# Performance work log

Hardware: AMD Instinct MI355X
Metric: run time of the kernel (lower is better)

The kernel has to match this reference:

```python
import jax, jax.numpy as jnp
import numpy as np
from jax import lax

B, H, W = 16, 512, 512
K, C, D = 64, 512, 256  # num_clusters, feature channels, descriptor_dim


def conv2d(x, w, b, stride, pad):
    y = lax.conv_general_dilated(x, w, (stride, stride), ((pad, pad), (pad, pad)),
                                 dimension_numbers=("NCHW", "OIHW", "NCHW"))
    return y + b[None, :, None, None]


def maxpool2(x):
    return lax.reduce_window(x, -jnp.inf, lax.max, (1, 1, 2, 2), (1, 1, 2, 2), "VALID")


def setup_inputs() -> dict:
    key = jax.random.key(0)
    ks = jax.random.split(key, 16)
    def rn(k, shape, fan_in):
        return jax.random.normal(k, shape, jnp.float32) * (1.0 / np.sqrt(fan_in))
    return {
        "x": jax.random.normal(ks[0], (B, 3, H, W), jnp.float32),
        "w1": rn(ks[1], (64, 3, 3, 3), 27), "b1": jnp.zeros((64,), jnp.float32),
        "w2": rn(ks[2], (128, 64, 3, 3), 576), "b2": jnp.zeros((128,), jnp.float32),
        "w3": rn(ks[3], (256, 128, 3, 3), 1152), "b3": jnp.zeros((256,), jnp.float32),
        "w4": rn(ks[4], (512, 256, 3, 3), 2304), "b4": jnp.zeros((512,), jnp.float32),
        "wv": rn(ks[5], (K, C), C), "bv": jnp.zeros((K,), jnp.float32),
        "centroids": jax.random.normal(ks[6], (K, C), jnp.float32),
        "fw1": rn(ks[7], (D, K * C), K * C), "fb1": jnp.zeros((D,), jnp.float32),
        "fw2": rn(ks[8], (D, D), D), "fb2": jnp.zeros((D,), jnp.float32),
    }


def reference(x, w1, b1, w2, b2, w3, b3, w4, b4, wv, bv, centroids, fw1, fb1, fw2, fb2):
    # conv backbone (SimpleGlobalDescriptor.backbone)
    h = jax.nn.relu(conv2d(x, w1, b1, 2, 1)); h = maxpool2(h)
    h = jax.nn.relu(conv2d(h, w2, b2, 2, 1)); h = maxpool2(h)
    h = jax.nn.relu(conv2d(h, w3, b3, 2, 1)); h = maxpool2(h)
    h = jax.nn.relu(conv2d(h, w4, b4, 2, 1))
    feats = jnp.mean(h, axis=(2, 3))  # AdaptiveAvgPool2d((1,1)) -> (B, C)
    # NetVLAD soft assignment: 1x1 conv + softmax over cluster dim
    logits = jnp.einsum("bc,kc->bk", feats, wv) + bv  # (B, K)
    a = jax.nn.softmax(logits, axis=1)  # spatial N == 1 after avgpool
    # fused VLAD: a[:,k] * (feats - centroids[k]) summed over N(=1)
    # == a (outer) feats - a[:,:,None] * centroids
    vlad = a[:, :, None] * (feats[:, None, :] - centroids[None, :, :])  # (B, K, C)
    v = vlad.reshape(B, K * C)
    # final descriptor MLP + L2 norm
    d = jax.nn.relu(v @ fw1.T + fb1) @ fw2.T + fb2
    d = d / jnp.linalg.norm(d, axis=1, keepdims=True)
    return d
```

## Files before the change

kernel.cpp:

```cpp
#include <hip/hip_runtime.h>
#include <hip/hip_bf16.h>

typedef unsigned short ushort_t;
typedef short bf16x8 __attribute__((ext_vector_type(8)));
typedef float f32x4 __attribute__((ext_vector_type(4)));

__device__ __forceinline__ ushort_t f2b(float f) {
    __hip_bfloat16 h = __float2bfloat16(f);
    return *reinterpret_cast<ushort_t*>(&h);
}
__device__ __forceinline__ float b2f(short v) {
    union { unsigned int u; float f; } cv;
    cv.u = ((unsigned int)(ushort_t)v) << 16;
    return cv.f;
}

__global__ __launch_bounds__(256) void k_packall(const float* __restrict__ w1,
                                                 const float* __restrict__ w2,
                                                 const float* __restrict__ w3,
                                                 const float* __restrict__ w4,
                                                 ushort_t* __restrict__ o1,
                                                 ushort_t* __restrict__ o2,
                                                 ushort_t* __restrict__ o3,
                                                 ushort_t* __restrict__ o4m) {
    const int bx = blockIdx.x;
    if (bx < 512) {
        const int co = bx;
        __shared__ float sw[2304];
        for (int i = threadIdx.x; i < 2304; i += 256) sw[i] = w4[(size_t)co * 2304 + i];
        __syncthreads();
        const int g = co >> 4, l15 = co & 15;
        for (int it = threadIdx.x; it < 288; it += 256) {
            const int kc = it >> 2, kg = it & 3;
            const int k0 = kc * 32 + kg * 8;
            const int tap = k0 >> 8, ci0 = k0 & 255;
            const int lane = kg * 16 + l15;
            ushort_t tmp[8];
#pragma unroll
            for (int j = 0; j < 8; ++j)
                tmp[j] = f2b(sw[(ci0 + j) * 9 + tap]);
            *(float4*)(o4m + ((size_t)(kc * 32 + g) * 64 + lane) * 8) = *(const float4*)tmp;
        }
    } else if (bx < 656) {
        const int slot = (bx - 512) * 256 + threadIdx.x;
        const int lane = slot & 63, g = (slot >> 6) & 15, kc = slot >> 10;
        const int k0 = kc * 32 + ((lane >> 4) << 3);
        const int tap = k0 >> 7, cib = k0 & 127;
        const int ky = tap >= 6 ? 2 : (tap >= 3 ? 1 : 0), kx = tap - ky * 3;
        const int co = g * 16 + (lane & 15);
#pragma unroll
        for (int j = 0; j < 8; ++j)
            o3[slot * 8 + j] = f2b(w3[((co * 128 + cib + j) * 3 + ky) * 3 + kx]);
    } else if (bx < 692) {
        const int slot = (bx - 656) * 256 + threadIdx.x;
        const int lane = slot & 63, g = (slot >> 6) & 7, kc = slot >> 9;
        const int k0 = kc * 32 + ((lane >> 4) << 3);
        const int tap = k0 >> 6, sb = k0 & 63;
        const int ky = tap >= 6 ? 2 : (tap >= 3 ? 1 : 0), kx = tap - ky * 3;
        const int co = g * 16 + (lane & 15);
#pragma unroll
        for (int j = 0; j < 8; ++j) {
            const int s = sb + j;
            const int ci = 16 * (s & 3) + (s >> 2);
            o2[slot * 8 + j] = f2b(w2[((co * 64 + ci) * 3 + ky) * 3 + kx]);
        }
    } else {
        const int slot = threadIdx.x;
        const int lane = slot & 63, nf = slot >> 6;
        const int co = nf * 16 + (lane & 15);
        const int kg = lane >> 4;
#pragma unroll
        for (int j = 0; j < 8; ++j) {
            const int k = kg * 8 + j;
            float v = 0.f;
            if (k < 24) {
                const int ky = k >> 3, q = k & 7;
                const int kx = q / 3, c = q - 3 * kx;
                v = w1[(co * 3 + c) * 9 + ky * 3 + kx];
            } else if (k < 27) {
                const int ky = k - 24;
                v = w1[(co * 3 + 2) * 9 + ky * 3 + 2];
            }
            o1[slot * 8 + j] = f2b(v);
        }
    }
}

__global__ __launch_bounds__(256) void k_conv1f(const float* __restrict__ x,
                                                const ushort_t* __restrict__ wpk1,
                                                const float* __restrict__ b1,
                                                ushort_t* __restrict__ y1) {
    const int rp = blockIdx.x, xh = blockIdx.y, b = blockIdx.z;
    const int tid = threadIdx.x;
    const int wid = tid >> 6, lane = tid & 63;
    const int l15 = lane & 15, kg = lane >> 4;

    __shared__ __align__(16) ushort_t sX[9 * 776];
    const float* xb = x + (size_t)b * 3 * 512 * 512;
    const int iy0 = 8 * rp - 1;
    const int ix0 = 256 * xh - 1;
#pragma unroll
    for (int c = 0; c < 3; ++c)
#pragma unroll
    for (int r = 0; r < 9; ++r) {
        const int iy = iy0 + r;
        const int ix = ix0 + tid;
        float v = 0.f;
        if (iy >= 0 && ix >= 0) v = xb[((size_t)c * 512 + iy) * 512 + ix];
        sX[r * 776 + tid * 3 + c] = f2b(v);
    }
    if (tid < 27) {
        const int c = tid / 9, r = tid - 9 * c;
        const int iy = iy0 + r, ix = ix0 + 256;
        float v = (iy >= 0) ? xb[((size_t)c * 512 + iy) * 512 + ix] : 0.f;
        sX[r * 776 + 256 * 3 + c] = f2b(v);
    }
    __syncthreads();

    const int gq = l15 >> 2;
    const int dy = (l15 >> 1) & 1, dx = l15 & 1;

    bf16x8 bF[4];
    float bias[4];
#pragma unroll
    for (int nf = 0; nf < 4; ++nf) {
        bF[nf] = *reinterpret_cast<const bf16x8*>(wpk1 + (size_t)(nf * 64 + lane) * 8);
        bias[nf] = b1[nf * 16 + l15];
    }
    const f32x4 z4 = {0.f, 0.f, 0.f, 0.f};

#pragma unroll 4
    for (int it = 0; it < 8; ++it) {
        const int fl = wid * 8 + it;
        const int g2 = fl * 4 + gq;
        const int pyl = g2 >> 6, pxl = g2 & 63;
        const int cr = 2 * pyl + dy;
        const int oxl = 2 * pxl + dx;
        bf16x8 aF;
        if (kg < 3) {
            const int ba = (2 * cr + kg) * 776 + 6 * oxl;
            const unsigned int* pu = (const unsigned int*)(sX + ba);
            union { unsigned int u[4]; bf16x8 v; } cvt;
            cvt.u[0] = pu[0]; cvt.u[1] = pu[1]; cvt.u[2] = pu[2]; cvt.u[3] = pu[3];
            aF = cvt.v;
        } else {
            const int b0 = 2 * cr * 776 + 6 * oxl + 8;
            aF = (bf16x8){0, 0, 0, 0, 0, 0, 0, 0};
            aF[0] = (short)sX[b0];
            aF[1] = (short)sX[b0 + 776];
            aF[2] = (short)sX[b0 + 1552];
        }
        f32x4 acc[4];
#pragma unroll
        for (int nf = 0; nf < 4; ++nf)
            acc[nf] = __builtin_amdgcn_mfma_f32_16x16x32_bf16(aF, bF[nf], z4, 0, 0, 0);
        const int g_out = fl * 4 + kg;
        const int pyo = g_out >> 6, pxo = xh * 64 + (g_out & 63);
        union { ushort_t u[4]; uint2 v; } pk;
#pragma unroll
        for (int nf = 0; nf < 4; ++nf) {
            float v = fmaxf(fmaxf(acc[nf][0], acc[nf][1]), fmaxf(acc[nf][2], acc[nf][3]));
            pk.u[nf] = f2b(fmaxf(v + bias[nf], 0.f));
        }
        *(uint2*)(y1 + ((size_t)(b * 128 + 2 * rp + pyo) * 128 + pxo) * 64 + 4 * l15) = pk.v;
    }
}

__global__ __launch_bounds__(256) void k_conv2s(const ushort_t* __restrict__ y1,
                                                const ushort_t* __restrict__ wpk2,
                                                const float* __restrict__ b2,
                                                ushort_t* __restrict__ y2) {
    const int b = blockIdx.z;
    const int xh = blockIdx.y;
    const int rp = blockIdx.x;
    const int tid = threadIdx.x;
    const int wid = tid >> 6, lane = tid & 63;
    const int l15 = lane & 15, kg = lane >> 4;

    __shared__ __align__(16) ushort_t sY[330 * 72];
    bf16x8* sYv = (bf16x8*)sY;

    const ushort_t* xb = y1 + (size_t)b * 128 * 128 * 64;
    const int iyb = 4 * rp - 1, ixb = 64 * xh - 1;
    for (int j = tid; j < 2640; j += 256) {
        const int q = j & 7;
        const int pc = j >> 3;
        const int cc = pc % 66, r = pc / 66;
        const int iy = iyb + r, ix = ixb + cc;
        bf16x8 v = {0, 0, 0, 0, 0, 0, 0, 0};
        if (iy >= 0 && ix >= 0 && ix < 128)
            v = *reinterpret_cast<const bf16x8*>(xb + ((size_t)iy * 128 + ix) * 64 + q * 8);
        sYv[pc * 9 + (q ^ ((pc >> 1) & 7))] = v;
    }
    __syncthreads();

    const f32x4 z4 = {0.f, 0.f, 0.f, 0.f};
    f32x4 acc[2][2][2];
#pragma unroll
    for (int i = 0; i < 2; ++i)
#pragma unroll
        for (int j = 0; j < 2; ++j) { acc[i][j][0] = z4; acc[i][j][1] = z4; }

#pragma unroll 1
    for (int tap = 0; tap < 9; ++tap) {
        const int ky = tap >= 6 ? 2 : (tap >= 3 ? 1 : 0), kx = tap - ky * 3;
#pragma unroll
        for (int h = 0; h < 2; ++h) {
            const int kc = tap * 2 + h;
            const int c8 = h * 4 + kg;
            bf16x8 aF[2][2];
#pragma unroll
            for (int oyi = 0; oyi < 2; ++oyi)
#pragma unroll
            for (int m2 = 0; m2 < 2; ++m2) {
                const int r = 2 * oyi + ky;
                const int cc = 2 * l15 + m2 * 32 + kx;
                const int pc = r * 66 + cc;
                aF[oyi][m2] = sYv[pc * 9 + (c8 ^ ((pc >> 1) & 7))];
            }
            bf16x8 bF[2];
#pragma unroll
            for (int nf = 0; nf < 2; ++nf)
                bF[nf] = *reinterpret_cast<const bf16x8*>(wpk2 + ((size_t)(kc * 8 + wid * 2 + nf) * 64 + lane) * 8);
#pragma unroll
            for (int oyi = 0; oyi < 2; ++oyi)
#pragma unroll
            for (int m2 = 0; m2 < 2; ++m2)
#pragma unroll
            for (int nf = 0; nf < 2; ++nf)
                acc[oyi][m2][nf] = __builtin_amdgcn_mfma_f32_16x16x32_bf16(aF[oyi][m2], bF[nf], acc[oyi][m2][nf], 0, 0, 0);
        }
    }
    const int kgx = lane >> 4;
#pragma unroll
    for (int nf = 0; nf < 2; ++nf) {
        const int co = wid * 32 + nf * 16 + l15;
        const float bias = b2[co];
#pragma unroll
        for (int m2 = 0; m2 < 2; ++m2)
#pragma unroll
            for (int p = 0; p < 2; ++p) {
                float v = fmaxf(fmaxf(acc[0][m2][nf][2 * p], acc[0][m2][nf][2 * p + 1]),
                                fmaxf(acc[1][m2][nf][2 * p], acc[1][m2][nf][2 * p + 1]));
                const int px = (xh * 2 + m2) * 8 + kgx * 2 + p;
                y2[((size_t)(b * 32 + rp) * 32 + px) * 128 + co] = f2b(fmaxf(v + bias, 0.f));
            }
    }
}

__global__ __launch_bounds__(256) void k_conv3m(const ushort_t* __restrict__ y2,
                                                const ushort_t* __restrict__ wpk3,
                                                const float* __restrict__ b3,
                                                ushort_t* __restrict__ y3) {
    const int gy = blockIdx.x, gn = blockIdx.y, b = blockIdx.z;
    const int oy0 = gy * 4;
    const int tid = threadIdx.x;
    const int wid = tid >> 6, lane = tid & 63;
    const int l15 = lane & 15, kl8 = (lane >> 4) << 3;
    const int g16 = gn * 4 + wid;
    const int co = g16 * 16 + l15;

    const ushort_t* xb = y2 + (size_t)b * 32 * 32 * 128;
    const f32x4 z4 = {0.f, 0.f, 0.f, 0.f};
    f32x4 acc[4] = {z4, z4, z4, z4};

#pragma unroll 1
    for (int tap = 0; tap < 9; ++tap) {
        const int ky = tap >= 6 ? 2 : (tap >= 3 ? 1 : 0), kx = tap - ky * 3;
        const int iyA = 2 * oy0 - 1 + ky;
        const int c = 2 * l15 - 1 + kx;
        const bool cok = (c >= 0);
#pragma unroll
        for (int h = 0; h < 4; ++h) {
            const int ci0 = h * 32;
            const int kc = tap * 4 + h;
            bf16x8 aF[4];
#pragma unroll
            for (int mf = 0; mf < 4; ++mf) {
                const int iy = iyA + 2 * mf;
                bf16x8 r = {0, 0, 0, 0, 0, 0, 0, 0};
                if (cok && iy >= 0) r = *reinterpret_cast<const bf16x8*>(xb + ((size_t)iy * 32 + c) * 128 + ci0 + kl8);
                aF[mf] = r;
            }
            const bf16x8 bF = *reinterpret_cast<const bf16x8*>(wpk3 + ((size_t)(kc * 16 + g16) * 64 + lane) * 8);
#pragma unroll
            for (int mf = 0; mf < 4; ++mf)
                acc[mf] = __builtin_amdgcn_mfma_f32_16x16x32_bf16(aF[mf], bF, acc[mf], 0, 0, 0);
        }
    }
    const int kg = lane >> 4;
    const float bias = b3[co];
#pragma unroll
    for (int mp = 0; mp < 2; ++mp) {
        const int py = gy * 2 + mp;
#pragma unroll
        for (int p = 0; p < 2; ++p) {
            float v = fmaxf(fmaxf(acc[2 * mp][2 * p], acc[2 * mp][2 * p + 1]),
                            fmaxf(acc[2 * mp + 1][2 * p], acc[2 * mp + 1][2 * p + 1]));
            const int px = kg * 2 + p;
            y3[((size_t)(b * 8 + py) * 8 + px) * 256 + co] = f2b(fmaxf(v + bias, 0.f));
        }
    }
}

__global__ __launch_bounds__(256) void k_conv4g(const ushort_t* __restrict__ y3,
                                                const ushort_t* __restrict__ wpk4m,
                                                const float* __restrict__ b4,
                                                float* __restrict__ feats) {
    const int g16 = blockIdx.x, b = blockIdx.y;
    const int tid = threadIdx.x, wid = tid >> 6, lane = tid & 63;
    const int l15 = lane & 15, kg = lane >> 4, kl8 = kg << 3;
    const int oy = l15 >> 2, ox = l15 & 3;
    const f32x4 z4 = {0.f, 0.f, 0.f, 0.f};
    f32x4 acc = z4;
    const ushort_t* yb = y3 + (size_t)b * 16384;
    const int kc0 = wid * 18;

#pragma unroll 3
    for (int i = 0; i < 18; ++i) {
        const int kc = kc0 + i;
        const int k0 = kc * 32 + kl8;
        const int tap = k0 >> 8, ci0 = k0 & 255;
        const int ky = tap / 3, kx = tap - 3 * (tap / 3);
        const int iy = 2 * oy - 1 + ky, ix = 2 * ox - 1 + kx;
        bf16x8 aF = {0, 0, 0, 0, 0, 0, 0, 0};
        if (iy >= 0 && ix >= 0)
            aF = *reinterpret_cast<const bf16x8*>(yb + ((iy * 8 + ix) << 8) + ci0);
        const bf16x8 bF = *reinterpret_cast<const bf16x8*>(wpk4m + ((size_t)(kc * 32 + g16) * 64 + lane) * 8);
        acc = __builtin_amdgcn_mfma_f32_16x16x32_bf16(aF, bF, acc, 0, 0, 0);
    }

    __shared__ f32x4 red[4][64];
    red[wid][lane] = acc;
    __syncthreads();
    if (wid == 0) {
        f32x4 t = red[0][lane];
        t = t + red[1][lane];
        t = t + red[2][lane];
        t = t + red[3][lane];
        const int co = g16 * 16 + l15;
        const float bias = b4[co];
        float s = fmaxf(t[0] + bias, 0.f) + fmaxf(t[1] + bias, 0.f)
                + fmaxf(t[2] + bias, 0.f) + fmaxf(t[3] + bias, 0.f);
        s += __shfl_xor(s, 16, 64);
        s += __shfl_xor(s, 32, 64);
        if (kg == 0) feats[b * 512 + co] = s * 0.0625f;
    }
}

__global__ __launch_bounds__(256) void k_head(const float* __restrict__ feats,
                                              const float* __restrict__ wv,
                                              const float* __restrict__ bv,
                                              const float* __restrict__ centroids,
                                              ushort_t* __restrict__ v) {
    const int b = blockIdx.x, sl8 = blockIdx.y;
    __shared__ float sf[512];
    __shared__ float sl[64];
    __shared__ float sa[64];
    for (int i = threadIdx.x; i < 512; i += 256) sf[i] = feats[b * 512 + i];
    __syncthreads();
    if (threadIdx.x < 64) {
        const int k = threadIdx.x;
        float s = bv[k];
        for (int c = 0; c < 512; ++c) s += sf[c] * wv[(size_t)k * 512 + c];
        sl[k] = s;
    }
    __syncthreads();
    if (threadIdx.x < 64) {
        const int k = threadIdx.x;
        float m = -1e30f;
        for (int i = 0; i < 64; ++i) m = fmaxf(m, sl[i]);
        float sum = 0.f;
        for (int i = 0; i < 64; ++i) sum += __expf(sl[i] - m);
        sa[k] = __expf(sl[k] - m) / sum;
    }
    __syncthreads();
    const int i4end = (sl8 + 1) * 4096;
    for (int i4 = sl8 * 4096 + threadIdx.x * 4; i4 < i4end; i4 += 1024) {
        const int k = i4 >> 9;
        const float a_ = sa[k];
        const float4 c4 = *(const float4*)(centroids + i4);
        const float4 f4 = *(const float4*)(&sf[i4 & 511]);
        union { ushort_t u[4]; uint2 w; } pk;
        pk.u[0] = f2b(a_ * (f4.x - c4.x));
        pk.u[1] = f2b(a_ * (f4.y - c4.y));
        pk.u[2] = f2b(a_ * (f4.z - c4.z));
        pk.u[3] = f2b(a_ * (f4.w - c4.w));
        *(uint2*)(v + (size_t)b * 32768 + i4) = pk.w;
    }
}

__global__ __launch_bounds__(256) void k_fc1m(const ushort_t* __restrict__ v,
                                              const float* __restrict__ fw1,
                                              float* __restrict__ part) {
    const int g16 = blockIdx.x, by = blockIdx.y;
    const int tid = threadIdx.x, wid = tid >> 6, lane = tid & 63;
    const int l15 = lane & 15, kg = lane >> 4;
    const f32x4 z4 = {0.f, 0.f, 0.f, 0.f};
    f32x4 acc = z4;
    const ushort_t* vrow = v + (size_t)l15 * 32768;
    const float* wrow = fw1 + (size_t)(g16 * 16 + l15) * 32768;
    const int kc0 = by * 16 + wid * 4;

#pragma unroll
    for (int i = 0; i < 4; ++i) {
        const int j0 = (kc0 + i) * 32 + kg * 8;
        const bf16x8 aF = *reinterpret_cast<const bf16x8*>(vrow + j0);
        const float4 wa = *(const float4*)(wrow + j0);
        const float4 wb = *(const float4*)(wrow + j0 + 4);
        bf16x8 bF;
        bF[0] = (short)f2b(wa.x); bF[1] = (short)f2b(wa.y);
        bF[2] = (short)f2b(wa.z); bF[3] = (short)f2b(wa.w);
        bF[4] = (short)f2b(wb.x); bF[5] = (short)f2b(wb.y);
        bF[6] = (short)f2b(wb.z); bF[7] = (short)f2b(wb.w);
        acc = __builtin_amdgcn_mfma_f32_16x16x32_bf16(aF, bF, acc, 0, 0, 0);
    }

    __shared__ f32x4 red[4][64];
    red[wid][lane] = acc;
    __syncthreads();
    if (wid == 0) {
        f32x4 t = red[0][lane];
        t = t + red[1][lane];
        t = t + red[2][lane];
        t = t + red[3][lane];
#pragma unroll
        for (int r = 0; r < 4; ++r)
            part[((size_t)by * 16 + (kg * 4 + r)) * 256 + g16 * 16 + l15] = t[r];
    }
}

__global__ __launch_bounds__(256) void k_fc2(const float* __restrict__ part,
                                             const float* __restrict__ fb1,
                                             const float* __restrict__ fw2,
                                             const float* __restrict__ fb2,
                                             float* __restrict__ out) {
    const int b = blockIdx.x;
    const int dd = threadIdx.x;
    __shared__ float sd[256];
    __shared__ float sq[256];
    float t = fb1[dd];
#pragma unroll 8
    for (int ks = 0; ks < 64; ++ks) t += part[((size_t)ks * 16 + b) * 256 + dd];
    sd[dd] = fmaxf(t, 0.f);
    __syncthreads();
    float s = fb2[dd];
    for (int j = 0; j < 256; ++j) s += sd[j] * fw2[(size_t)dd * 256 + j];
    sq[dd] = s * s;
    __syncthreads();
    for (int off = 128; off >= 1; off >>= 1) {
        if (dd < off) sq[dd] += sq[dd + off];
        __syncthreads();
    }
    const float inv = rsqrtf(sq[0]);
    out[b * 256 + dd] = s * inv;
}

extern "C" void kernel_launch(void* const* d_in, const int* in_sizes, int n_in,
                              void* d_out, int out_size, void* d_ws, size_t ws_size,
                              hipStream_t stream) {
    const float* x    = (const float*)d_in[0];
    const float* w1   = (const float*)d_in[1];
    const float* b1   = (const float*)d_in[2];
    const float* w2   = (const float*)d_in[3];
    const float* b2   = (const float*)d_in[4];
    const float* w3   = (const float*)d_in[5];
    const float* b3   = (const float*)d_in[6];
    const float* w4   = (const float*)d_in[7];
    const float* b4   = (const float*)d_in[8];
    const float* wv   = (const float*)d_in[9];
    const float* bv   = (const float*)d_in[10];
    const float* cen  = (const float*)d_in[11];
    const float* fw1  = (const float*)d_in[12];
    const float* fb1  = (const float*)d_in[13];
    const float* fw2  = (const float*)d_in[14];
    const float* fb2  = (const float*)d_in[15];
    float* out = (float*)d_out;

    char* p = (char*)d_ws;
    ushort_t* y1    = (ushort_t*)p; p += 33554432;
    ushort_t* wpk2  = (ushort_t*)p; p += 147456;
    ushort_t* wpk3  = (ushort_t*)p; p += 589824;
    ushort_t* wpk4m = (ushort_t*)p; p += 2359296;
    ushort_t* wpk1  = (ushort_t*)p; p += 4096;
    ushort_t* y2    = (ushort_t*)p; p += 4194304;
    ushort_t* y3    = (ushort_t*)p; p += 524288;
    float*    feats = (float*)p;    p += 32768;
    ushort_t* vbuf  = (ushort_t*)p; p += 1048576;
    float*    part  = (float*)p;    p += 1048576;

    k_packall<<<693, 256, 0, stream>>>(w1, w2, w3, w4, wpk1, wpk2, wpk3, wpk4m);
    k_conv1f<<<dim3(64, 2, 16), 256, 0, stream>>>(x, wpk1, b1, y1);
    k_conv2s<<<dim3(32, 2, 16), 256, 0, stream>>>(y1, wpk2, b2, y2);
    k_conv3m<<<dim3(4, 4, 16), 256, 0, stream>>>(y2, wpk3, b3, y3);
    k_conv4g<<<dim3(32, 16), 256, 0, stream>>>(y3, wpk4m, b4, feats);
    k_head<<<dim3(16, 8), 256, 0, stream>>>(feats, wv, bv, cen, vbuf);
    k_fc1m<<<dim3(16, 64), 256, 0, stream>>>(vbuf, fw1, part);
    k_fc2<<<16, 256, 0, stream>>>(part, fb1, fw2, fb2, out);
}
```

Baseline: 111.8 us.

## Fuse conv1 and conv2 into one kernel with pooled tile kept in LDS

Merges the conv1+pool and conv2+pool kernels into a single kernel. Each block computes a haloed conv1 tile directly into shared memory and then runs conv2 from it, so the 32 MB bf16 y1 intermediate is never written to or read back from global memory. The cost is recomputing the overlapping halo regions of conv1 per block and a more complex indexing and padding scheme. The block count also doubles while each block does less conv2 work.

After: 131.6 us. +17.7%, slower.

```diff
diff --git a/kernel.cpp b/kernel.cpp
--- a/kernel.cpp
+++ b/kernel.cpp
@@ -86,120 +86,111 @@
     }
 }
 
-__global__ __launch_bounds__(256) void k_conv1f(const float* __restrict__ x,
-                                                const ushort_t* __restrict__ wpk1,
-                                                const float* __restrict__ b1,
-                                                ushort_t* __restrict__ y1) {
-    const int rp = blockIdx.x, xh = blockIdx.y, b = blockIdx.z;
+__global__ __launch_bounds__(256) void k_c12f(const float* __restrict__ x,
+                                              const ushort_t* __restrict__ wpk1,
+                                              const ushort_t* __restrict__ wpk2,
+                                              const float* __restrict__ b1,
+                                              const float* __restrict__ b2,
+                                              ushort_t* __restrict__ y2) {
+    const int rp = blockIdx.x, xq = blockIdx.y, b = blockIdx.z;
     const int tid = threadIdx.x;
     const int wid = tid >> 6, lane = tid & 63;
     const int l15 = lane & 15, kg = lane >> 4;
 
-    __shared__ __align__(16) ushort_t sX[9 * 776];
+    __shared__ __align__(16) ushort_t sX[21 * 412];
+    __shared__ __align__(16) ushort_t sY[170 * 72];
+    bf16x8* sYv = (bf16x8*)sY;
+
     const float* xb = x + (size_t)b * 3 * 512 * 512;
-    const int iy0 = 8 * rp - 1;
-    const int ix0 = 256 * xh - 1;
-#pragma unroll
-    for (int c = 0; c < 3; ++c)
-#pragma unroll
-    for (int r = 0; r < 9; ++r) {
-        const int iy = iy0 + r;
-        const int ix = ix0 + tid;
-        float v = 0.f;
-        if (iy >= 0 && ix >= 0) v = xb[((size_t)c * 512 + iy) * 512 + ix];
-        sX[r * 776 + tid * 3 + c] = f2b(v);
-    }
-    if (tid < 27) {
-        const int c = tid / 9, r = tid - 9 * c;
-        const int iy = iy0 + r, ix = ix0 + 256;
-        float v = (iy >= 0) ? xb[((size_t)c * 512 + iy) * 512 + ix] : 0.f;
-        sX[r * 776 + 256 * 3 + c] = f2b(v);
-    }
-    __syncthreads();
-
-    const int gq = l15 >> 2;
-    const int dy = (l15 >> 1) & 1, dx = l15 & 1;
-
-    bf16x8 bF[4];
-    float bias[4];
-#pragma unroll
-    for (int nf = 0; nf < 4; ++nf) {
-        bF[nf] = *reinterpret_cast<const bf16x8*>(wpk1 + (size_t)(nf * 64 + lane) * 8);
-        bias[nf] = b1[nf * 16 + l15];
-    }
+    const int rowbase = 16 * rp - 5;
+    const int colbase = 128 * xq - 5;
+#pragma unroll
+    for (int c = 0; c < 3; ++c) {
+        for (int pass = 0; pass < 12; ++pass) {
+            const int idx = pass * 256 + tid;
+            if (idx < 2877) {
+                const int row = idx / 137;
+                const int col = idx - 137 * row;
+                const int rg = rowbase + row, cg = colbase + col;
+                float v = 0.f;
+                if (rg >= 0 && cg >= 0 && cg < 512)
+                    v = xb[((size_t)c * 512 + rg) * 512 + cg];
+                sX[row * 412 + col * 3 + c] = f2b(v);
+            }
+        }
+    }
+    __syncthreads();
+
+    {
+        bf16x8 bF1[4];
+        float bias1[4];
+#pragma unroll
+        for (int nf = 0; nf < 4; ++nf) {
+            bF1[nf] = *reinterpret_cast<const bf16x8*>(wpk1 + (size_t)(nf * 64 + lane) * 8);
+            bias1[nf] = b1[nf * 16 + l15];
+        }
+        const f32x4 z4 = {0.f, 0.f, 0.f, 0.f};
+        const int qi = l15 & 3;
+        const int dy = qi >> 1, dx2 = qi & 1;
+        const int pgl = l15 >> 2;
+
+#pragma unroll 2
+        for (int it = 0; it < 11; ++it) {
+            const int f = wid * 11 + it;
+            if (f <= 42) {
+                int p = f * 4 + pgl;
+                if (p > 169) p = 169;
+                const int r = p / 34;
+                const int u = p - 34 * r;
+                const int xr0 = 4 * r + 2 * dy;
+                const int cof = (4 * u + 2 * dx2) * 3;
+                bf16x8 aF;
+                if (kg < 3) {
+                    const int off = (xr0 + kg) * 412 + cof;
+                    const unsigned int* pu = (const unsigned int*)(sX + off);
+                    union { unsigned int u4[4]; bf16x8 v; } cvt;
+                    cvt.u4[0] = pu[0]; cvt.u4[1] = pu[1]; cvt.u4[2] = pu[2]; cvt.u4[3] = pu[3];
+                    aF = cvt.v;
+                } else {
+                    const int b0 = xr0 * 412 + cof + 8;
+                    aF = (bf16x8){0, 0, 0, 0, 0, 0, 0, 0};
+                    aF[0] = (short)sX[b0];
+                    aF[1] = (short)sX[b0 + 412];
+                    aF[2] = (short)sX[b0 + 824];
+                }
+                f32x4 acc[4];
+#pragma unroll
+                for (int nf = 0; nf < 4; ++nf)
+                    acc[nf] = __builtin_amdgcn_mfma_f32_16x16x32_bf16(aF, bF1[nf], z4, 0, 0, 0);
+                const int p2 = f * 4 + kg;
+                if (p2 <= 169) {
+                    const int r2 = p2 / 34;
+                    const int u2 = p2 - 34 * r2;
+                    const bool valid = !(rp == 0 && r2 == 0) && !(xq == 0 && u2 == 0)
+                                     && !(xq == 3 && u2 == 33);
+                    union { ushort_t u4[4]; uint2 w; } pk;
+                    if (valid) {
+#pragma unroll
+                        for (int nf = 0; nf < 4; ++nf) {
+                            float v = fmaxf(fmaxf(acc[nf][0], acc[nf][1]),
+                                            fmaxf(acc[nf][2], acc[nf][3]));
+                            pk.u4[nf] = f2b(fmaxf(v + bias1[nf], 0.f));
+                        }
+                    } else {
+                        pk.u4[0] = 0; pk.u4[1] = 0; pk.u4[2] = 0; pk.u4[3] = 0;
+                    }
+                    const int q = (l15 >> 1) ^ ((p2 >> 1) & 7);
+                    *(uint2*)(sY + p2 * 72 + q * 8 + (l15 & 1) * 4) = pk.w;
+                }
+            }
+        }
+    }
+    __syncthreads();
+
     const f32x4 z4 = {0.f, 0.f, 0.f, 0.f};
-
-#pragma unroll 4
-    for (int it = 0; it < 8; ++it) {
-        const int fl = wid * 8 + it;
-        const int g2 = fl * 4 + gq;
-        const int pyl = g2 >> 6, pxl = g2 & 63;
-        const int cr = 2 * pyl + dy;
-        const int oxl = 2 * pxl + dx;
-        bf16x8 aF;
-        if (kg < 3) {
-            const int ba = (2 * cr + kg) * 776 + 6 * oxl;
-            const unsigned int* pu = (const unsigned int*)(sX + ba);
-            union { unsigned int u[4]; bf16x8 v; } cvt;
-            cvt.u[0] = pu[0]; cvt.u[1] = pu[1]; cvt.u[2] = pu[2]; cvt.u[3] = pu[3];
-            aF = cvt.v;
-        } else {
-            const int b0 = 2 * cr * 776 + 6 * oxl + 8;
-            aF = (bf16x8){0, 0, 0, 0, 0, 0, 0, 0};
-            aF[0] = (short)sX[b0];
-            aF[1] = (short)sX[b0 + 776];
-            aF[2] = (short)sX[b0 + 1552];
-        }
-        f32x4 acc[4];
-#pragma unroll
-        for (int nf = 0; nf < 4; ++nf)
-            acc[nf] = __builtin_amdgcn_mfma_f32_16x16x32_bf16(aF, bF[nf], z4, 0, 0, 0);
-        const int g_out = fl * 4 + kg;
-        const int pyo = g_out >> 6, pxo = xh * 64 + (g_out & 63);
-        union { ushort_t u[4]; uint2 v; } pk;
-#pragma unroll
-        for (int nf = 0; nf < 4; ++nf) {
-            float v = fmaxf(fmaxf(acc[nf][0], acc[nf][1]), fmaxf(acc[nf][2], acc[nf][3]));
-            pk.u[nf] = f2b(fmaxf(v + bias[nf], 0.f));
-        }
-        *(uint2*)(y1 + ((size_t)(b * 128 + 2 * rp + pyo) * 128 + pxo) * 64 + 4 * l15) = pk.v;
-    }
-}
-
-__global__ __launch_bounds__(256) void k_conv2s(const ushort_t* __restrict__ y1,
-                                                const ushort_t* __restrict__ wpk2,
-                                                const float* __restrict__ b2,
-                                                ushort_t* __restrict__ y2) {
-    const int b = blockIdx.z;
-    const int xh = blockIdx.y;
-    const int rp = blockIdx.x;
-    const int tid = threadIdx.x;
-    const int wid = tid >> 6, lane = tid & 63;
-    const int l15 = lane & 15, kg = lane >> 4;
-
-    __shared__ __align__(16) ushort_t sY[330 * 72];
-    bf16x8* sYv = (bf16x8*)sY;
-
-    const ushort_t* xb = y1 + (size_t)b * 128 * 128 * 64;
-    const int iyb = 4 * rp - 1, ixb = 64 * xh - 1;
-    for (int j = tid; j < 2640; j += 256) {
-        const int q = j & 7;
-        const int pc = j >> 3;
-        const int cc = pc % 66, r = pc / 66;
-        const int iy = iyb + r, ix = ixb + cc;
-        bf16x8 v = {0, 0, 0, 0, 0, 0, 0, 0};
-        if (iy >= 0 && ix >= 0 && ix < 128)
-            v = *reinterpret_cast<const bf16x8*>(xb + ((size_t)iy * 128 + ix) * 64 + q * 8);
-        sYv[pc * 9 + (q ^ ((pc >> 1) & 7))] = v;
-    }
-    __syncthreads();
-
-    const f32x4 z4 = {0.f, 0.f, 0.f, 0.f};
-    f32x4 acc[2][2][2];
-#pragma unroll
-    for (int i = 0; i < 2; ++i)
-#pragma unroll
-        for (int j = 0; j < 2; ++j) { acc[i][j][0] = z4; acc[i][j][1] = z4; }
+    f32x4 acc[2][2];
+#pragma unroll
+    for (int i = 0; i < 2; ++i) { acc[i][0] = z4; acc[i][1] = z4; }
 
 #pragma unroll 1
     for (int tap = 0; tap < 9; ++tap) {
@@ -208,15 +199,11 @@
         for (int h = 0; h < 2; ++h) {
             const int kc = tap * 2 + h;
             const int c8 = h * 4 + kg;
-            bf16x8 aF[2][2];
-#pragma unroll
-            for (int oyi = 0; oyi < 2; ++oyi)
-#pragma unroll
-            for (int m2 = 0; m2 < 2; ++m2) {
-                const int r = 2 * oyi + ky;
-                const int cc = 2 * l15 + m2 * 32 + kx;
-                const int pc = r * 66 + cc;
-                aF[oyi][m2] = sYv[pc * 9 + (c8 ^ ((pc >> 1) & 7))];
+            bf16x8 aF[2];
+#pragma unroll
+            for (int oyi = 0; oyi < 2; ++oyi) {
+                const int pc = (2 * oyi + ky) * 34 + 2 * l15 + kx;
+                aF[oyi] = sYv[pc * 9 + (c8 ^ ((pc >> 1) & 7))];
             }
             bf16x8 bF[2];
 #pragma unroll
@@ -225,26 +212,21 @@
 #pragma unroll
             for (int oyi = 0; oyi < 2; ++oyi)
 #pragma unroll
-            for (int m2 = 0; m2 < 2; ++m2)
-#pragma unroll
             for (int nf = 0; nf < 2; ++nf)
-                acc[oyi][m2][nf] = __builtin_amdgcn_mfma_f32_16x16x32_bf16(aF[oyi][m2], bF[nf], acc[oyi][m2][nf], 0, 0, 0);
-        }
-    }
-    const int kgx = lane >> 4;
+                acc[oyi][nf] = __builtin_amdgcn_mfma_f32_16x16x32_bf16(aF[oyi], bF[nf], acc[oyi][nf], 0, 0, 0);
+        }
+    }
 #pragma unroll
     for (int nf = 0; nf < 2; ++nf) {
         const int co = wid * 32 + nf * 16 + l15;
         const float bias = b2[co];
 #pragma unroll
-        for (int m2 = 0; m2 < 2; ++m2)
-#pragma unroll
-            for (int p = 0; p < 2; ++p) {
-                float v = fmaxf(fmaxf(acc[0][m2][nf][2 * p], acc[0][m2][nf][2 * p + 1]),
-                                fmaxf(acc[1][m2][nf][2 * p], acc[1][m2][nf][2 * p + 1]));
-                const int px = (xh * 2 + m2) * 8 + kgx * 2 + p;
-                y2[((size_t)(b * 32 + rp) * 32 + px) * 128 + co] = f2b(fmaxf(v + bias, 0.f));
-            }
+        for (int p = 0; p < 2; ++p) {
+            float v = fmaxf(fmaxf(acc[0][nf][2 * p], acc[0][nf][2 * p + 1]),
+                            fmaxf(acc[1][nf][2 * p], acc[1][nf][2 * p + 1]));
+            const int px = xq * 8 + kg * 2 + p;
+            y2[((size_t)(b * 32 + rp) * 32 + px) * 128 + co] = f2b(fmaxf(v + bias, 0.f));
+        }
     }
 }
 
@@ -478,7 +460,6 @@
     float* out = (float*)d_out;
 
     char* p = (char*)d_ws;
-    ushort_t* y1    = (ushort_t*)p; p += 33554432;
     ushort_t* wpk2  = (ushort_t*)p; p += 147456;
     ushort_t* wpk3  = (ushort_t*)p; p += 589824;
     ushort_t* wpk4m = (ushort_t*)p; p += 2359296;
@@ -490,8 +471,7 @@
     float*    part  = (float*)p;    p += 1048576;
 
     k_packall<<<693, 256, 0, stream>>>(w1, w2, w3, w4, wpk1, wpk2, wpk3, wpk4m);
-    k_conv1f<<<dim3(64, 2, 16), 256, 0, stream>>>(x, wpk1, b1, y1);
-    k_conv2s<<<dim3(32, 2, 16), 256, 0, stream>>>(y1, wpk2, b2, y2);
+    k_c12f<<<dim3(32, 4, 16), 256, 0, stream>>>(x, wpk1, wpk2, b1, b2, y2);
     k_conv3m<<<dim3(4, 4, 16), 256, 0, stream>>>(y2, wpk3, b3, y3);
     k_conv4g<<<dim3(32, 16), 256, 0, stream>>>(y3, wpk4m, b4, feats);
     k_head<<<dim3(16, 8), 256, 0, stream>>>(feats, wv, bv, cen, vbuf);
```
